# Kernel optimization log

Hardware: AMD Instinct MI355X
Metric: run time of the kernel (lower is better)

The kernel has to match this reference:

```python
import jax, jax.numpy as jnp
import numpy as np

N = 50000          # node_num
E = 800000         # edges before self-loops (avg degree 16)
H = 1              # heads
C = 64             # out_channel (== embedding dim)
D_IN = 64          # in_channel
NEG_SLOPE = 0.2    # GraphLayer leaky_relu negative_slope
BN_EPS = 1e-5


def setup_inputs() -> dict:
    key = jax.random.key(0)
    ks = jax.random.split(key, 12)
    x = jax.random.normal(ks[0], (N, D_IN), jnp.float32)
    # random edges with no self-loops (forward removes then re-adds self-loops)
    src = jax.random.randint(ks[1], (E,), 0, N, dtype=jnp.int32)
    off = jax.random.randint(ks[2], (E,), 1, N, dtype=jnp.int32)
    dst = (src + off) % N
    edge_index = jnp.stack([src, dst])            # [2, E], row0=j (source), row1=i (target)
    embedding = jax.random.normal(ks[3], (N, C), jnp.float32)
    sc = 1.0 / np.sqrt(D_IN)
    W = jax.random.normal(ks[4], (H * C, D_IN), jnp.float32) * sc   # lin.weight
    att_i = jax.random.normal(ks[5], (1, H, C), jnp.float32) * 0.1
    att_j = jax.random.normal(ks[6], (1, H, C), jnp.float32) * 0.1
    att_em_i = jax.random.normal(ks[7], (1, H, C), jnp.float32) * 0.1
    att_em_j = jax.random.normal(ks[8], (1, H, C), jnp.float32) * 0.1
    bias = jnp.zeros((C,), jnp.float32)           # GraphLayer bias (concat=False)
    bn_gamma = jnp.ones((C,), jnp.float32)
    bn_beta = jnp.zeros((C,), jnp.float32)
    return {"x": x, "edge_index": edge_index, "embedding": embedding, "W": W,
            "att_i": att_i, "att_j": att_j, "att_em_i": att_em_i, "att_em_j": att_em_j,
            "bias": bias, "bn_gamma": bn_gamma, "bn_beta": bn_beta}


def reference(x, edge_index, embedding, W, att_i, att_j, att_em_i, att_em_j, bias, bn_gamma, bn_beta):
    n = x.shape[0]
    xl = (x @ W.T).reshape(n, H, C)                       # lin(x) -> [N, H, C]
    # add self-loops (input edges have none)
    loops = jnp.arange(n, dtype=edge_index.dtype)
    src = jnp.concatenate([edge_index[0], loops])         # j
    dst = jnp.concatenate([edge_index[1], loops])         # i (aggregation target)
    x_j = xl[src]                                         # [E', H, C]
    x_i = xl[dst]
    emb_i = embedding[dst][:, None, :]                    # [E', 1, C] broadcast over heads
    emb_j = embedding[src][:, None, :]
    # alpha = <cat(x_i, emb_i), cat(att_i, att_em_i)> + <cat(x_j, emb_j), cat(att_j, att_em_j)>
    a = ((x_i * att_i).sum(-1) + (emb_i * att_em_i).sum(-1)
         + (x_j * att_j).sum(-1) + (emb_j * att_em_j).sum(-1))   # [E', H]
    a = jnp.where(a >= 0, a, NEG_SLOPE * a)               # leaky_relu(0.2)
    # segment softmax over target nodes
    amax = jax.ops.segment_max(a, dst, num_segments=n)    # every node has a self-loop
    ea = jnp.exp(a - amax[dst])
    denom = jax.ops.segment_sum(ea, dst, num_segments=n)
    alpha = ea / (denom[dst] + 1e-16)                     # [E', H]
    msg = x_j * alpha[..., None]                          # [E', H, C]
    out = jax.ops.segment_sum(msg, dst, num_segments=n)   # [N, H, C]
    out = out.mean(axis=1) + bias                         # concat=False -> head mean
    # BatchNorm1d (training mode: batch stats) + ReLU
    mu = out.mean(axis=0)
    var = ((out - mu) ** 2).mean(axis=0)
    out = (out - mu) * jax.lax.rsqrt(var + BN_EPS) * bn_gamma + bn_beta
    return jnp.maximum(out, 0.0)
```

## Files before the change

kernel.cpp:

```cpp
#include <hip/hip_runtime.h>
#include <hip/hip_bf16.h>

#define NEG_SLOPE 0.2f
#define BN_EPS 1e-5f
#define CAP 48

__global__ void __launch_bounds__(256, 4)
k_lin_scatter(const float* __restrict__ x, const float* __restrict__ W,
              const float* __restrict__ emb,
              const float* __restrict__ att_i, const float* __restrict__ att_j,
              const float* __restrict__ att_em_i, const float* __restrict__ att_em_j,
              const int* __restrict__ src, const int* __restrict__ dst, int E,
              int* __restrict__ cursor, unsigned short* __restrict__ bucket,
              __hip_bfloat16* __restrict__ xlh, float* __restrict__ s_i,
              float* __restrict__ s_j, int N) {
    int tid = threadIdx.x;
    int gtid = blockIdx.x * blockDim.x + tid;
    int gsz = gridDim.x * blockDim.x;

    for (int e = gtid; e < E; e += gsz) {
        int d = dst[e];
        int p = atomicAdd(&cursor[d], 1);
        if (p < CAP) bucket[(size_t)d * CAP + p] = (unsigned short)src[e];
    }

    int lane = tid & 63;
    const float4* Wv = (const float4*)(W + (size_t)lane * 64);
    float4 w0 = Wv[0], w1 = Wv[1], w2 = Wv[2], w3 = Wv[3];
    float4 w4 = Wv[4], w5 = Wv[5], w6 = Wv[6], w7 = Wv[7];
    float4 w8 = Wv[8], w9 = Wv[9], w10 = Wv[10], w11 = Wv[11];
    float4 w12 = Wv[12], w13 = Wv[13], w14 = Wv[14], w15 = Wv[15];
    float ai = att_i[lane], aj = att_j[lane];
    float aei = att_em_i[lane], aej = att_em_j[lane];

    int gwave = gtid >> 6;
    int nwaves = gsz >> 6;
    for (int r = gwave; r < N; r += nwaves) {
        int ru = __builtin_amdgcn_readfirstlane(r);
        const float4* xrow = (const float4*)(x + (size_t)ru * 64);
        float acc = 0.f;
#define STEP(q, wq) { float4 xv = xrow[q]; \
        acc = fmaf(xv.x, wq.x, acc); acc = fmaf(xv.y, wq.y, acc); \
        acc = fmaf(xv.z, wq.z, acc); acc = fmaf(xv.w, wq.w, acc); }
        STEP(0, w0) STEP(1, w1) STEP(2, w2) STEP(3, w3)
        STEP(4, w4) STEP(5, w5) STEP(6, w6) STEP(7, w7)
        STEP(8, w8) STEP(9, w9) STEP(10, w10) STEP(11, w11)
        STEP(12, w12) STEP(13, w13) STEP(14, w14) STEP(15, w15)
#undef STEP
        xlh[(size_t)ru * 64 + lane] = __float2bfloat16(acc);
        float e = emb[(size_t)ru * 64 + lane];
        float vi = fmaf(acc, ai, e * aei);
        float vj = fmaf(acc, aj, e * aej);
#pragma unroll
        for (int o = 32; o; o >>= 1) {
            vi += __shfl_xor(vi, o, 64);
            vj += __shfl_xor(vj, o, 64);
        }
        if (lane == 0) { s_i[ru] = vi; s_j[ru] = vj; }
    }
}

__global__ void __launch_bounds__(256, 8)
k_aggregate(const __hip_bfloat16* __restrict__ xlh, const float* __restrict__ s_i,
            const float* __restrict__ s_j, const int* __restrict__ cursor,
            const unsigned short* __restrict__ bucket, const float* __restrict__ bias,
            float* __restrict__ pre, int N) {
    int lane = threadIdx.x & 63;
    int w = threadIdx.x >> 6;
    int i = blockIdx.x * 4 + w;
    if (i >= N) return;

    int deg = cursor[i];
    deg = deg < CAP ? deg : CAP;
    size_t base = (size_t)i * CAP;
    float sii = s_i[i];
    float a_self = sii + s_j[i];
    a_self = a_self >= 0.f ? a_self : NEG_SLOPE * a_self;

    int jreg = 0;
    float areg = -1e30f;
    if (lane < deg) {
        jreg = (int)bucket[base + lane];
        float a = sii + s_j[jreg];
        areg = a >= 0.f ? a : NEG_SLOPE * a;
    }
    float m = fmaxf(a_self, areg);
#pragma unroll
    for (int o = 32; o; o >>= 1) m = fmaxf(m, __shfl_xor(m, o, 64));
    float wreg = (lane < deg) ? __expf(areg - m) : 0.f;
    float dsum = wreg;
#pragma unroll
    for (int o = 32; o; o >>= 1) dsum += __shfl_xor(dsum, o, 64);
    float w_self = __expf(a_self - m);
    float denom = dsum + w_self + 1e-16f;

    float acc = w_self * (float)xlh[(size_t)i * 64 + lane];
    int wbits = __float_as_int(wreg);
    int e = 0;
#define GL(k) int j##k = __builtin_amdgcn_readlane(jreg, e + k); \
              float u##k = __int_as_float(__builtin_amdgcn_readlane(wbits, e + k)); \
              float v##k = (float)xlh[(size_t)j##k * 64 + lane];
#define FM(k) acc = fmaf(u##k, v##k, acc);
    for (; e + 15 < deg; e += 16) {
        GL(0) GL(1) GL(2) GL(3) GL(4) GL(5) GL(6) GL(7)
        GL(8) GL(9) GL(10) GL(11) GL(12) GL(13) GL(14) GL(15)
        FM(0) FM(1) FM(2) FM(3) FM(4) FM(5) FM(6) FM(7)
        FM(8) FM(9) FM(10) FM(11) FM(12) FM(13) FM(14) FM(15)
    }
    for (; e + 7 < deg; e += 8) {
        GL(0) GL(1) GL(2) GL(3) GL(4) GL(5) GL(6) GL(7)
        FM(0) FM(1) FM(2) FM(3) FM(4) FM(5) FM(6) FM(7)
    }
#undef GL
#undef FM
    for (; e < deg; ++e) {
        int j = __builtin_amdgcn_readlane(jreg, e);
        float wv = __int_as_float(__builtin_amdgcn_readlane(wbits, e));
        acc = fmaf(wv, (float)xlh[(size_t)j * 64 + lane], acc);
    }
    pre[(size_t)i * 64 + lane] = acc / denom + bias[lane];
}

__global__ void k_stats(const float* __restrict__ pre, int N, float* __restrict__ sums) {
    int lane = threadIdx.x & 63, w = threadIdx.x >> 6;
    int gwave = blockIdx.x * (blockDim.x >> 6) + w;
    int stride = gridDim.x * (blockDim.x >> 6);
    float s = 0.f, q = 0.f;
    for (int r = gwave; r < N; r += stride) {
        float v = pre[(size_t)r * 64 + lane];
        s += v;
        q = fmaf(v, v, q);
    }
    __shared__ float ls[4][64], lq[4][64];
    ls[w][lane] = s;
    lq[w][lane] = q;
    __syncthreads();
    if (w == 0) {
        s = ls[0][lane] + ls[1][lane] + ls[2][lane] + ls[3][lane];
        q = lq[0][lane] + lq[1][lane] + lq[2][lane] + lq[3][lane];
        atomicAdd(&sums[lane], s);
        atomicAdd(&sums[64 + lane], q);
    }
}

__global__ void __launch_bounds__(256, 4)
k_norm(const float* __restrict__ pre, const float* __restrict__ sums,
       const float* __restrict__ gamma, const float* __restrict__ beta,
       float* __restrict__ out, int N, int total4) {
    __shared__ float sc_sh[64], sh_sh[64];
    int tid = threadIdx.x;
    if (tid < 64) {
        float invN = 1.f / (float)N;
        float mu = sums[tid] * invN;
        float var = sums[64 + tid] * invN - mu * mu;
        float sc = gamma[tid] * rsqrtf(var + BN_EPS);
        sc_sh[tid] = sc;
        sh_sh[tid] = beta[tid] - mu * sc;
    }
    __syncthreads();
    for (int i = blockIdx.x * blockDim.x + tid; i < total4; i += gridDim.x * blockDim.x) {
        int c = (i & 15) * 4;
        float4 p = ((const float4*)pre)[i];
        float4 r;
        r.x = fmaxf(fmaf(p.x, sc_sh[c + 0], sh_sh[c + 0]), 0.f);
        r.y = fmaxf(fmaf(p.y, sc_sh[c + 1], sh_sh[c + 1]), 0.f);
        r.z = fmaxf(fmaf(p.z, sc_sh[c + 2], sh_sh[c + 2]), 0.f);
        r.w = fmaxf(fmaf(p.w, sc_sh[c + 3], sh_sh[c + 3]), 0.f);
        ((float4*)out)[i] = r;
    }
}

extern "C" void kernel_launch(void* const* d_in, const int* in_sizes, int n_in,
                              void* d_out, int out_size, void* d_ws, size_t ws_size,
                              hipStream_t stream) {
    const float* x        = (const float*)d_in[0];
    const int*   ei       = (const int*)d_in[1];
    const float* emb      = (const float*)d_in[2];
    const float* W        = (const float*)d_in[3];
    const float* att_i    = (const float*)d_in[4];
    const float* att_j    = (const float*)d_in[5];
    const float* att_em_i = (const float*)d_in[6];
    const float* att_em_j = (const float*)d_in[7];
    const float* bias     = (const float*)d_in[8];
    const float* gamma    = (const float*)d_in[9];
    const float* beta     = (const float*)d_in[10];

    int N = in_sizes[0] / 64;
    int E = in_sizes[1] / 2;
    const int* srcv = ei;
    const int* dstv = ei + E;

    char* ws = (char*)d_ws;
    size_t o = 0;
    auto alloc = [&](size_t bytes) -> char* {
        char* p = ws + o;
        o += bytes;
        o = (o + 255) & ~(size_t)255;
        return p;
    };
    __hip_bfloat16* xlh   = (__hip_bfloat16*)alloc((size_t)N * 64 * 2);
    float* s_i            = (float*)alloc((size_t)N * 4);
    float* s_j            = (float*)alloc((size_t)N * 4);
    unsigned short* bucket = (unsigned short*)alloc((size_t)N * CAP * 2);
    char*  zbase  = alloc((size_t)N * 4 + 128 * 4);
    int*   cursor = (int*)zbase;
    float* sums   = (float*)(zbase + (size_t)N * 4);
    float* pre    = (float*)d_out;

    hipMemsetAsync(zbase, 0, (size_t)N * 4 + 128 * 4, stream);

    k_lin_scatter<<<2048, 256, 0, stream>>>(x, W, emb, att_i, att_j, att_em_i, att_em_j,
                                            srcv, dstv, E, cursor, bucket,
                                            xlh, s_i, s_j, N);
    k_aggregate<<<(N + 3) / 4, 256, 0, stream>>>(xlh, s_i, s_j, cursor, bucket,
                                                 bias, pre, N);
    k_stats<<<256, 256, 0, stream>>>(pre, N, sums);
    int total4 = N * 16;
    k_norm<<<512, 256, 0, stream>>>(pre, sums, gamma, beta, (float*)d_out, N, total4);
}
```

Before: 206.0 us.

## Use bf16 MFMA for node linear layer and partition edge scatter by XCD

The per-row FMA matrix-vector loop is replaced with bf16 16x16x32 MFMA tiles, where each wave computes 16 nodes. The attention dot products are now reduced within 16-lane groups. The edge bucketing pass is restructured so that each group of 8 blocks scans one edge slice, and each block only handles destinations whose bits match its block index mod 8. This is meant to keep the cursor atomics and bucket writes local to one L2 partition. The cost is that the dst array is read 8 times, and x and W are rounded to bf16 before the matmul.

```diff
diff --git a/kernel.cpp b/kernel.cpp
--- a/kernel.cpp
+++ b/kernel.cpp
@@ -5,58 +5,104 @@
 #define BN_EPS 1e-5f
 #define CAP 48
 
+typedef __attribute__((ext_vector_type(8))) short bf16x8;
+typedef __attribute__((ext_vector_type(4))) float f32x4;
+
+__device__ __forceinline__ bf16x8 pk8(float4 a, float4 b) {
+    union { __hip_bfloat16 h; short s; } u;
+    bf16x8 r;
+    u.h = __float2bfloat16(a.x); r[0] = u.s;
+    u.h = __float2bfloat16(a.y); r[1] = u.s;
+    u.h = __float2bfloat16(a.z); r[2] = u.s;
+    u.h = __float2bfloat16(a.w); r[3] = u.s;
+    u.h = __float2bfloat16(b.x); r[4] = u.s;
+    u.h = __float2bfloat16(b.y); r[5] = u.s;
+    u.h = __float2bfloat16(b.z); r[6] = u.s;
+    u.h = __float2bfloat16(b.w); r[7] = u.s;
+    return r;
+}
+
 __global__ void __launch_bounds__(256, 4)
-k_lin_scatter(const float* __restrict__ x, const float* __restrict__ W,
-              const float* __restrict__ emb,
-              const float* __restrict__ att_i, const float* __restrict__ att_j,
-              const float* __restrict__ att_em_i, const float* __restrict__ att_em_j,
-              const int* __restrict__ src, const int* __restrict__ dst, int E,
-              int* __restrict__ cursor, unsigned short* __restrict__ bucket,
-              __hip_bfloat16* __restrict__ xlh, float* __restrict__ s_i,
-              float* __restrict__ s_j, int N) {
-    int tid = threadIdx.x;
-    int gtid = blockIdx.x * blockDim.x + tid;
-    int gsz = gridDim.x * blockDim.x;
-
-    for (int e = gtid; e < E; e += gsz) {
-        int d = dst[e];
-        int p = atomicAdd(&cursor[d], 1);
-        if (p < CAP) bucket[(size_t)d * CAP + p] = (unsigned short)src[e];
-    }
-
-    int lane = tid & 63;
-    const float4* Wv = (const float4*)(W + (size_t)lane * 64);
-    float4 w0 = Wv[0], w1 = Wv[1], w2 = Wv[2], w3 = Wv[3];
-    float4 w4 = Wv[4], w5 = Wv[5], w6 = Wv[6], w7 = Wv[7];
-    float4 w8 = Wv[8], w9 = Wv[9], w10 = Wv[10], w11 = Wv[11];
-    float4 w12 = Wv[12], w13 = Wv[13], w14 = Wv[14], w15 = Wv[15];
-    float ai = att_i[lane], aj = att_j[lane];
-    float aei = att_em_i[lane], aej = att_em_j[lane];
-
-    int gwave = gtid >> 6;
-    int nwaves = gsz >> 6;
-    for (int r = gwave; r < N; r += nwaves) {
-        int ru = __builtin_amdgcn_readfirstlane(r);
-        const float4* xrow = (const float4*)(x + (size_t)ru * 64);
-        float acc = 0.f;
-#define STEP(q, wq) { float4 xv = xrow[q]; \
-        acc = fmaf(xv.x, wq.x, acc); acc = fmaf(xv.y, wq.y, acc); \
-        acc = fmaf(xv.z, wq.z, acc); acc = fmaf(xv.w, wq.w, acc); }
-        STEP(0, w0) STEP(1, w1) STEP(2, w2) STEP(3, w3)
-        STEP(4, w4) STEP(5, w5) STEP(6, w6) STEP(7, w7)
-        STEP(8, w8) STEP(9, w9) STEP(10, w10) STEP(11, w11)
-        STEP(12, w12) STEP(13, w13) STEP(14, w14) STEP(15, w15)
-#undef STEP
-        xlh[(size_t)ru * 64 + lane] = __float2bfloat16(acc);
-        float e = emb[(size_t)ru * 64 + lane];
-        float vi = fmaf(acc, ai, e * aei);
-        float vj = fmaf(acc, aj, e * aej);
-#pragma unroll
-        for (int o = 32; o; o >>= 1) {
-            vi += __shfl_xor(vi, o, 64);
-            vj += __shfl_xor(vj, o, 64);
+k_scatter_mfma(const float* __restrict__ x, const float* __restrict__ W,
+               const float* __restrict__ emb,
+               const float* __restrict__ att_i, const float* __restrict__ att_j,
+               const float* __restrict__ att_em_i, const float* __restrict__ att_em_j,
+               const int* __restrict__ src, const int* __restrict__ dst, int E,
+               int* __restrict__ cursor, unsigned short* __restrict__ bucket,
+               __hip_bfloat16* __restrict__ xlh, float* __restrict__ s_i,
+               float* __restrict__ s_j, int N) {
+    {
+        int myx = blockIdx.x & 7;
+        int slice = blockIdx.x >> 3;
+        int per = (E + 255) / 256;
+        int e0 = slice * per;
+        int e1 = e0 + per; if (e1 > E) e1 = E;
+        for (int e = e0 + threadIdx.x; e < e1; e += 256) {
+            int d = dst[e];
+            if (((d >> 6) & 7) == myx) {
+                int p = atomicAdd(&cursor[d], 1);
+                if (p < CAP) bucket[(size_t)d * CAP + p] = (unsigned short)src[e];
+            }
         }
-        if (lane == 0) { s_i[ru] = vi; s_j[ru] = vj; }
+    }
+
+    int gw = blockIdx.x * 4 + (threadIdx.x >> 6);
+    int ntiles = (N + 15) >> 4;
+    if (gw >= ntiles) return;
+    int lane = threadIdx.x & 63;
+    int m = lane & 15;
+    int q = lane >> 4;
+    int r0 = gw * 16;
+
+    const float* xrow = x + (size_t)(r0 + m) * 64;
+    float4 xa0 = *(const float4*)(xrow + q * 8);
+    float4 xa1 = *(const float4*)(xrow + q * 8 + 4);
+    float4 xb0 = *(const float4*)(xrow + 32 + q * 8);
+    float4 xb1 = *(const float4*)(xrow + 32 + q * 8 + 4);
+    bf16x8 A0 = pk8(xa0, xa1);
+    bf16x8 A1 = pk8(xb0, xb1);
+
+    f32x4 acc0 = {0.f, 0.f, 0.f, 0.f}, acc1 = acc0, acc2 = acc0, acc3 = acc0;
+#define CTILE(ct, accv) { \
+        const float* wrow = W + (size_t)(ct * 16 + m) * 64; \
+        float4 wb0 = *(const float4*)(wrow + q * 8); \
+        float4 wb1 = *(const float4*)(wrow + q * 8 + 4); \
+        float4 wb2 = *(const float4*)(wrow + 32 + q * 8); \
+        float4 wb3 = *(const float4*)(wrow + 32 + q * 8 + 4); \
+        bf16x8 B0 = pk8(wb0, wb1); \
+        bf16x8 B1 = pk8(wb2, wb3); \
+        accv = __builtin_amdgcn_mfma_f32_16x16x32_bf16(A0, B0, accv, 0, 0, 0); \
+        accv = __builtin_amdgcn_mfma_f32_16x16x32_bf16(A1, B1, accv, 0, 0, 0); }
+    CTILE(0, acc0) CTILE(1, acc1) CTILE(2, acc2) CTILE(3, acc3)
+#undef CTILE
+
+    float ati0 = att_i[m],      ati1 = att_i[16 + m],      ati2 = att_i[32 + m],      ati3 = att_i[48 + m];
+    float atj0 = att_j[m],      atj1 = att_j[16 + m],      atj2 = att_j[32 + m],      atj3 = att_j[48 + m];
+    float aei0 = att_em_i[m],   aei1 = att_em_i[16 + m],   aei2 = att_em_i[32 + m],   aei3 = att_em_i[48 + m];
+    float aej0 = att_em_j[m],   aej1 = att_em_j[16 + m],   aej2 = att_em_j[32 + m],   aej3 = att_em_j[48 + m];
+#pragma unroll
+    for (int reg = 0; reg < 4; ++reg) {
+        int r = r0 + q * 4 + reg;
+        if (r < N) {
+            float v0 = acc0[reg], v1 = acc1[reg], v2 = acc2[reg], v3 = acc3[reg];
+            __hip_bfloat16* xo = xlh + (size_t)r * 64 + m;
+            xo[0]  = __float2bfloat16(v0);
+            xo[16] = __float2bfloat16(v1);
+            xo[32] = __float2bfloat16(v2);
+            xo[48] = __float2bfloat16(v3);
+            const float* er = emb + (size_t)r * 64 + m;
+            float e0 = er[0], e1 = er[16], e2 = er[32], e3 = er[48];
+            float pi = v0 * ati0 + v1 * ati1 + v2 * ati2 + v3 * ati3
+                     + e0 * aei0 + e1 * aei1 + e2 * aei2 + e3 * aei3;
+            float pj = v0 * atj0 + v1 * atj1 + v2 * atj2 + v3 * atj3
+                     + e0 * aej0 + e1 * aej1 + e2 * aej2 + e3 * aej3;
+#pragma unroll
+            for (int o = 1; o < 16; o <<= 1) {
+                pi += __shfl_xor(pi, o, 64);
+                pj += __shfl_xor(pj, o, 64);
+            }
+            if (m == 0) { s_i[r] = pi; s_j[r] = pj; }
+        }
     }
 }
 
@@ -84,14 +130,14 @@
         float a = sii + s_j[jreg];
         areg = a >= 0.f ? a : NEG_SLOPE * a;
     }
-    float m = fmaxf(a_self, areg);
-#pragma unroll
-    for (int o = 32; o; o >>= 1) m = fmaxf(m, __shfl_xor(m, o, 64));
-    float wreg = (lane < deg) ? __expf(areg - m) : 0.f;
+    float mx = fmaxf(a_self, areg);
+#pragma unroll
+    for (int o = 32; o; o >>= 1) mx = fmaxf(mx, __shfl_xor(mx, o, 64));
+    float wreg = (lane < deg) ? __expf(areg - mx) : 0.f;
     float dsum = wreg;
 #pragma unroll
     for (int o = 32; o; o >>= 1) dsum += __shfl_xor(dsum, o, 64);
-    float w_self = __expf(a_self - m);
+    float w_self = __expf(a_self - mx);
     float denom = dsum + w_self + 1e-16f;
 
     float acc = w_self * (float)xlh[(size_t)i * 64 + lane];
@@ -198,9 +244,9 @@
         o = (o + 255) & ~(size_t)255;
         return p;
     };
-    __hip_bfloat16* xlh   = (__hip_bfloat16*)alloc((size_t)N * 64 * 2);
-    float* s_i            = (float*)alloc((size_t)N * 4);
-    float* s_j            = (float*)alloc((size_t)N * 4);
+    __hip_bfloat16* xlh    = (__hip_bfloat16*)alloc((size_t)N * 64 * 2);
+    float* s_i             = (float*)alloc((size_t)N * 4);
+    float* s_j             = (float*)alloc((size_t)N * 4);
     unsigned short* bucket = (unsigned short*)alloc((size_t)N * CAP * 2);
     char*  zbase  = alloc((size_t)N * 4 + 128 * 4);
     int*   cursor = (int*)zbase;
@@ -209,9 +255,9 @@
 
     hipMemsetAsync(zbase, 0, (size_t)N * 4 + 128 * 4, stream);
 
-    k_lin_scatter<<<2048, 256, 0, stream>>>(x, W, emb, att_i, att_j, att_em_i, att_em_j,
-                                            srcv, dstv, E, cursor, bucket,
-                                            xlh, s_i, s_j, N);
+    k_scatter_mfma<<<2048, 256, 0, stream>>>(x, W, emb, att_i, att_j, att_em_i,
+                                             att_em_j, srcv, dstv, E, cursor, bucket,
+                                             xlh, s_i, s_j, N);
     k_aggregate<<<(N + 3) / 4, 256, 0, stream>>>(xlh, s_i, s_j, cursor, bucket,
                                                  bias, pre, N);
     k_stats<<<256, 256, 0, stream>>>(pre, N, sums);
```

Result: faster. 199.2 us (-3.3%).
